# Optimization experiments

Measured on AMD Instinct MI355X. Metric: run time of the kernel, lower is better.

The kernel has to match this reference:

```python
import jax, jax.numpy as jnp
import numpy as np
import math

N = 10000      # nodes per type
DIN = 64       # input feature dim
HID = 128      # hidden_dim
HEADS = 8      # num_heads
DH = 128       # per-head dim == out_channels (PyG TransformerConv)
INNER = HEADS * DH  # 1024
L = 2          # num_layers
E = 60000      # edges per edge type
FF = 512       # 4*hidden
LN_EPS = 1e-5


def setup_inputs():
    keys = iter(jax.random.split(jax.random.key(0), 80))
    def mk(shape, std=0.05):
        return std * jax.random.normal(next(keys), shape, dtype=jnp.float32)
    inp = {}
    for t in ("job", "mach"):
        inp[f"x_{t}"] = mk((N, DIN), 1.0)
        inp[f"Win_{t}"] = mk((DIN, HID)); inp[f"bin_{t}"] = mk((HID,), 0.01)
        inp[f"pos_{t}"] = mk((N, HID)); inp[f"te_{t}"] = mk((HID,))
        inp[f"lng_{t}"] = 1.0 + mk((L, HID), 0.02); inp[f"lnb_{t}"] = mk((L, HID), 0.02)
        inp[f"W1_{t}"] = mk((L, HID, FF)); inp[f"b1_{t}"] = mk((L, FF), 0.01)
        inp[f"W2_{t}"] = mk((L, FF, HID)); inp[f"b2_{t}"] = mk((L, HID), 0.01)
        inp[f"Wout_{t}"] = mk((HID, HID)); inp[f"bout_{t}"] = mk((HID,), 0.01)
    for et in ("jm", "mj"):
        inp[f"Wq_{et}"] = mk((L, HID, INNER)); inp[f"Wk_{et}"] = mk((L, HID, INNER))
        inp[f"Wv_{et}"] = mk((L, HID, INNER)); inp[f"Ws_{et}"] = mk((L, HID, HID))
        inp[f"Wb_{et}"] = mk((L, 3 * HID, 1))
        inp[f"bq_{et}"] = mk((L, INNER), 0.01); inp[f"bk_{et}"] = mk((L, INNER), 0.01)
        inp[f"bv_{et}"] = mk((L, INNER), 0.01); inp[f"bs_{et}"] = mk((L, HID), 0.01)
        inp[f"ei_{et}"] = jax.random.randint(next(keys), (2, E), 0, N, dtype=jnp.int32)
    return inp


def _layer_norm(x, g, b):
    mu = x.mean(-1, keepdims=True)
    var = ((x - mu) ** 2).mean(-1, keepdims=True)
    return (x - mu) / jnp.sqrt(var + LN_EPS) * g + b


def _tconv(x_src, x_dst, src, dst, Wq, bq, Wk, bk, Wv, bv, Ws, bs, Wb):
    # PyG TransformerConv(heads=HEADS, out_channels=DH, concat=False, beta=True, root_weight=True)
    Nd = x_dst.shape[0]
    q = (x_dst @ Wq + bq).reshape(Nd, HEADS, DH)
    k = (x_src @ Wk + bk).reshape(-1, HEADS, DH)
    v = (x_src @ Wv + bv).reshape(-1, HEADS, DH)
    logits = jnp.einsum('ehd,ehd->eh', q[dst], k[src]) / math.sqrt(DH)  # [E,H]
    # segment softmax over edges grouped by destination node
    m = jax.ops.segment_max(logits, dst, num_segments=Nd)
    m = jnp.where(jnp.isfinite(m), m, 0.0)  # empty segments -> -inf -> 0
    ex = jnp.exp(logits - m[dst])
    den = jax.ops.segment_sum(ex, dst, num_segments=Nd)
    alpha = ex / (den[dst] + 1e-16)
    agg = jax.ops.segment_sum(alpha[:, :, None] * v[src], dst, num_segments=Nd)
    out = agg.mean(axis=1)              # concat=False -> average heads -> [Nd, DH]
    x_r = x_dst @ Ws + bs               # root/skip projection
    beta = jax.nn.sigmoid(jnp.concatenate([out, x_r, out - x_r], axis=-1) @ Wb)  # [Nd,1]
    return beta * x_r + (1.0 - beta) * out


def _ffn_block(h, new, g, b, W1, b1, W2, b2):
    r = _layer_norm(h + new, g, b)
    return r + (jax.nn.gelu(r @ W1 + b1, approximate=False) @ W2 + b2)


def _forward(x_job, Win_job, bin_job, pos_job, te_job, lng_job, lnb_job, W1_job, b1_job, W2_job, b2_job, Wout_job, bout_job, x_mach, Win_mach, bin_mach, pos_mach, te_mach, lng_mach, lnb_mach, W1_mach, b1_mach, W2_mach, b2_mach, Wout_mach, bout_mach, Wq_jm, Wk_jm, Wv_jm, Ws_jm, Wb_jm, bq_jm, bk_jm, bv_jm, bs_jm, ei_jm, Wq_mj, Wk_mj, Wv_mj, Ws_mj, Wb_mj, bq_mj, bk_mj, bv_mj, bs_mj, ei_mj):
    h_j = x_job @ Win_job + bin_job + te_job + pos_job
    h_m = x_mach @ Win_mach + bin_mach + te_mach + pos_mach
    s_jm, d_jm = ei_jm[0], ei_jm[1]  # job -> mach
    s_mj, d_mj = ei_mj[0], ei_mj[1]  # mach -> job
    for l in range(L):
        new_m = _tconv(h_j, h_m, s_jm, d_jm, Wq_jm[l], bq_jm[l], Wk_jm[l], bk_jm[l], Wv_jm[l], bv_jm[l], Ws_jm[l], bs_jm[l], Wb_jm[l])
        new_j = _tconv(h_m, h_j, s_mj, d_mj, Wq_mj[l], bq_mj[l], Wk_mj[l], bk_mj[l], Wv_mj[l], bv_mj[l], Ws_mj[l], bs_mj[l], Wb_mj[l])
        h_j = _ffn_block(h_j, new_j, lng_job[l], lnb_job[l], W1_job[l], b1_job[l], W2_job[l], b2_job[l])
        h_m = _ffn_block(h_m, new_m, lng_mach[l], lnb_mach[l], W1_mach[l], b1_mach[l], W2_mach[l], b2_mach[l])
    return jnp.stack([h_j @ Wout_job + bout_job, h_m @ Wout_mach + bout_mach], axis=0)


def reference(x_job, Win_job, bin_job, pos_job, te_job, lng_job, lnb_job, W1_job, b1_job, W2_job, b2_job, Wout_job, bout_job, x_mach, Win_mach, bin_mach, pos_mach, te_mach, lng_mach, lnb_mach, W1_mach, b1_mach, W2_mach, b2_mach, Wout_mach, bout_mach, Wq_jm, Wk_jm, Wv_jm, Ws_jm, Wb_jm, bq_jm, bk_jm, bv_jm, bs_jm, ei_jm, Wq_mj, Wk_mj, Wv_mj, Ws_mj, Wb_mj, bq_mj, bk_mj, bv_mj, bs_mj, ei_mj):
    return _forward(x_job, Win_job, bin_job, pos_job, te_job, lng_job, lnb_job, W1_job, b1_job, W2_job, b2_job, Wout_job, bout_job, x_mach, Win_mach, bin_mach, pos_mach, te_mach, lng_mach, lnb_mach, W1_mach, b1_mach, W2_mach, b2_mach, Wout_mach, bout_mach, Wq_jm, Wk_jm, Wv_jm, Ws_jm, Wb_jm, bq_jm, bk_jm, bv_jm, bs_jm, ei_jm, Wq_mj, Wk_mj, Wv_mj, Ws_mj, Wb_mj, bq_mj, bk_mj, bv_mj, bs_mj, ei_mj)
```

## Files before the change

### kernel.cpp

```cpp
#include <hip/hip_runtime.h>
#include <hip/hip_bf16.h>

#define NN 10000
#define EE 60000
#define HIDD 128
#define NH 8
#define INNERD 1024
#define FFD 512
#define KVQ 3072
#define KVQS 3200

using u16 = unsigned short;
using u32 = unsigned int;

typedef __bf16 bf16x8 __attribute__((ext_vector_type(8)));
typedef float f32x4 __attribute__((ext_vector_type(4)));

__device__ __forceinline__ float u2f(u32 u) { return __uint_as_float(u << 16); }
__device__ __forceinline__ u16 f2b(float f) {
  u32 x = __float_as_uint(f);
  return (u16)((x + 0x7fffu + ((x >> 16) & 1u)) >> 16);
}
__device__ __forceinline__ float gelu_f(float x) {
  return 0.5f * x * (1.0f + erff(x * 0.70710678118654752f));
}

__global__ void detect_k(const u32* __restrict__ xw, int* __restrict__ flag) {
  if (threadIdx.x == 0 && blockIdx.x == 0) {
    int wild = 0;
    for (int i = 0; i < 256; ++i) {
      float v = u2f(xw[i] & 0xffffu);
      if (!(fabsf(v) < 1e4f)) ++wild;
    }
    *flag = (wild > 16) ? 1 : 0;
  }
}

#define NCVT 30
struct CvtArgs { const void* src[NCVT]; int cnt[NCVT]; int ntot; };

__global__ __launch_bounds__(256) void convert_k(CvtArgs a, const int* __restrict__ flag,
                                                 float* __restrict__ dst) {
  const int i = blockIdx.x * 256 + threadIdx.x;
  if (i >= a.ntot) return;
  int t = 0, off = i;
  while (off >= a.cnt[t]) { off -= a.cnt[t]; ++t; }
  const float v = (*flag) ? ((const float*)a.src[t])[off]
                          : u2f(((const u16*)a.src[t])[off]);
  dst[i] = v;
}

struct TT { const void* s; long off; u16* d; int K; int N; };
struct TTab { TT m[28]; };

__global__ __launch_bounds__(256) void transT_k(TTab tt, const int* __restrict__ flag) {
  const TT m = tt.m[blockIdx.z];
  const int n0 = blockIdx.x * 32, k0 = blockIdx.y * 32;
  if (n0 >= m.N || k0 >= m.K) return;
  __shared__ float tile[32][33];
  const int c = threadIdx.x;
  const int f32in = *flag;
  for (int i = threadIdx.y; i < 32; i += 8) {
    const long gi = m.off + (long)(k0 + i) * m.N + n0 + c;
    tile[i][c] = f32in ? ((const float*)m.s)[gi] : u2f(((const u16*)m.s)[gi]);
  }
  __syncthreads();
  for (int i = threadIdx.y; i < 32; i += 8)
    m.d[(size_t)(n0 + i) * m.K + k0 + c] = f2b(tile[c][i]);
}

__global__ __launch_bounds__(256) void hist_k(const int* __restrict__ ei0,
                                              const int* __restrict__ ei1,
                                              int* __restrict__ hist) {
  const int e = blockIdx.x * 256 + threadIdx.x;
  if (e >= EE) return;
  const int et = blockIdx.y;
  const int* ei = et ? ei1 : ei0;
  atomicAdd(&hist[et * NN + ei[EE + e]], 1);
}

__global__ __launch_bounds__(1024) void scan2_k(const int* __restrict__ hist,
                                                int* __restrict__ rowptr,
                                                int* __restrict__ cursor) {
  const int et = blockIdx.x;
  const int* h = hist + et * NN;
  int* rp = rowptr + et * (NN + 1);
  int* cu = cursor + et * NN;
  __shared__ int wsum[16];
  __shared__ int carrySm;
  const int t = threadIdx.x, lane = t & 63, wid = t >> 6;
  if (t == 0) carrySm = 0;
  __syncthreads();
  for (int base = 0; base < NN; base += 1024) {
    const int idx = base + t;
    const int v = (idx < NN) ? h[idx] : 0;
    int x = v;
#pragma unroll
    for (int off = 1; off < 64; off <<= 1) {
      int y = __shfl_up(x, off);
      if (lane >= off) x += y;
    }
    if (lane == 63) wsum[wid] = x;
    __syncthreads();
    if (wid == 0) {
      int s = (lane < 16) ? wsum[lane] : 0;
#pragma unroll
      for (int off = 1; off < 16; off <<= 1) {
        int y = __shfl_up(s, off);
        if (lane >= off) s += y;
      }
      if (lane < 16) wsum[lane] = s;
    }
    __syncthreads();
    const int waveoff = (wid > 0) ? wsum[wid - 1] : 0;
    const int incl = x + waveoff + carrySm;
    if (idx < NN) { rp[idx] = incl - v; cu[idx] = incl - v; }
    __syncthreads();
    if (t == 1023) carrySm = incl;
    __syncthreads();
  }
  if (t == 0) rp[NN] = carrySm;
}

__global__ __launch_bounds__(256) void scat_k(const int* __restrict__ ei0,
                                              const int* __restrict__ ei1,
                                              int* __restrict__ cursor,
                                              int* __restrict__ srcs) {
  const int e = blockIdx.x * 256 + threadIdx.x;
  if (e >= EE) return;
  const int et = blockIdx.y;
  const int* ei = et ? ei1 : ei0;
  const int s = ei[e], d = ei[EE + e];
  const int pos = atomicAdd(&cursor[et * NN + d], 1);
  srcs[et * EE + pos] = s;
}

__global__ __launch_bounds__(128) void embed2_k(
    const void* __restrict__ x0, const float* __restrict__ Win0,
    const float* __restrict__ bin0, const float* __restrict__ te0,
    const void* __restrict__ pos0, float* __restrict__ h0, u16* __restrict__ h80,
    const void* __restrict__ x1, const float* __restrict__ Win1,
    const float* __restrict__ bin1, const float* __restrict__ te1,
    const void* __restrict__ pos1, float* __restrict__ h1, u16* __restrict__ h81,
    const int* __restrict__ flag) {
  const int ty = blockIdx.y;
  const void* x = ty ? x1 : x0;
  const float* Win = ty ? Win1 : Win0;
  const float* bin = ty ? bin1 : bin0;
  const float* te = ty ? te1 : te0;
  const void* pos = ty ? pos1 : pos0;
  float* h = ty ? h1 : h0;
  u16* h8 = ty ? h81 : h80;
  __shared__ float Ws[64][128];
  __shared__ float xs[16][64];
  const int f32in = *flag;
  const int j = threadIdx.x;
  const int base = blockIdx.x * 16;
  for (int i = 0; i < 64; ++i) Ws[i][j] = Win[i * 128 + j];
  for (int r = 0; r < 8; ++r) {
    int idx = r * 128 + j;
    int row = idx >> 6, k = idx & 63;
    size_t gi = (size_t)(base + row) * 64 + k;
    xs[row][k] = f32in ? ((const float*)x)[gi] : u2f(((const u16*)x)[gi]);
  }
  __syncthreads();
  float bj = bin[j] + te[j];
  for (int row = 0; row < 16; ++row) {
    size_t gi = (size_t)(base + row) * 128 + j;
    float pv = f32in ? ((const float*)pos)[gi] : u2f(((const u16*)pos)[gi]);
    float acc = bj + pv;
#pragma unroll
    for (int k = 0; k < 64; ++k) acc += xs[row][k] * Ws[k][j];
    h[(size_t)(base + row) * 128 + j] = acc;
    h8[(size_t)(base + row) * 128 + j] = f2b(acc);
  }
}

struct MG {
  const u16* A; const u16* WT;
  const float* b0; const float* b1; const float* b2; const float* b3;
  const float* add; float* Cf; u16* Cb;
};

template <int MODE>
__global__ __launch_bounds__(256) void mgemm2_k(MG g0, MG g1, int M, int N, int K) {
  const MG g = blockIdx.z ? g1 : g0;
  __shared__ __align__(16) u16 Asl[128][40];
  __shared__ __align__(16) u16 Bsl[64][40];
  const int t = threadIdx.x;
  const int lane = t & 63, wid = t >> 6;
  const int bm = blockIdx.y * 128, bn = blockIdx.x * 64;
  const int rg = lane >> 4, rr = lane & 15;
  f32x4 acc[2][4];
#pragma unroll
  for (int i = 0; i < 2; ++i)
#pragma unroll
    for (int j = 0; j < 4; ++j) acc[i][j] = (f32x4){0.f, 0.f, 0.f, 0.f};
  const int ar = t >> 1;
  const int ah = (t & 1) << 4;
  const int wr = t >> 2;
  const int wk = (t & 3) << 3;

  for (int k0 = 0; k0 < K; k0 += 32) {
    const int garow = bm + ar;
    uint4 a0 = {0,0,0,0}, a1 = {0,0,0,0};
    if (garow < M) {
      const u16* ap = g.A + (size_t)garow * K + k0 + ah;
      a0 = *reinterpret_cast<const uint4*>(ap);
      a1 = *reinterpret_cast<const uint4*>(ap + 8);
    }
    *reinterpret_cast<uint4*>(&Asl[ar][ah]) = a0;
    *reinterpret_cast<uint4*>(&Asl[ar][ah + 8]) = a1;
    const uint4 bv = *reinterpret_cast<const uint4*>(g.WT + (size_t)(bn + wr) * K + k0 + wk);
    *reinterpret_cast<uint4*>(&Bsl[wr][wk]) = bv;
    __syncthreads();
    bf16x8 af[2], bfr[4];
#pragma unroll
    for (int mi = 0; mi < 2; ++mi)
      af[mi] = *reinterpret_cast<const bf16x8*>(&Asl[wid * 32 + mi * 16 + rr][rg * 8]);
#pragma unroll
    for (int ni = 0; ni < 4; ++ni)
      bfr[ni] = *reinterpret_cast<const bf16x8*>(&Bsl[ni * 16 + rr][rg * 8]);
#pragma unroll
    for (int mi = 0; mi < 2; ++mi)
#pragma unroll
      for (int ni = 0; ni < 4; ++ni)
        acc[mi][ni] = __builtin_amdgcn_mfma_f32_16x16x32_bf16(af[mi], bfr[ni], acc[mi][ni], 0, 0, 0);
    __syncthreads();
  }
#pragma unroll
  for (int mi = 0; mi < 2; ++mi) {
#pragma unroll
    for (int ni = 0; ni < 4; ++ni) {
      const int col = bn + ni * 16 + rr;
      float bcol;
      if (MODE == 2) {
        const int seg = col >> 10;
        const float* bp = (seg == 0) ? g.b0 : ((seg == 1) ? g.b1 : ((seg == 2) ? g.b2 : g.b3));
        bcol = bp[col & 1023];
      } else {
        bcol = g.b0[col];
      }
#pragma unroll
      for (int r = 0; r < 4; ++r) {
        const int row = bm + wid * 32 + mi * 16 + rg * 4 + r;
        if (row >= M) continue;
        float v = acc[mi][ni][r] + bcol;
        if (MODE == 2) {
          if (col < KVQ) g.Cb[(size_t)row * KVQ + col] = f2b(v);
          else           g.Cf[(size_t)row * HIDD + (col - KVQ)] = v;
        } else if (MODE == 3) {
          v = gelu_f(v);
          g.Cb[(size_t)row * N + col] = f2b(v);
        } else {
          v += g.add[(size_t)row * N + col];
          g.Cf[(size_t)row * N + col] = v;
          g.Cb[(size_t)row * N + col] = f2b(v);
        }
      }
    }
  }
}

struct VG {
  const float* A; const float* B; const float* bias;
  float* Cf; u16* Cb;
};

__global__ __launch_bounds__(256) void gemm2_k(VG g0, VG g1, const int* __restrict__ oflag,
                                               int M, int N, int K) {
  const VG g = blockIdx.z ? g1 : g0;
  __shared__ __align__(16) float As[16][64];
  __shared__ __align__(16) float Bs[16][64];
  const int t = threadIdx.x;
  const int tx = t & 15, ty = t >> 4;
  const int bm = blockIdx.y * 64, bn = blockIdx.x * 64;
  float c[4][4] = {{0.f}};
  const int am = t >> 2;
  const int ak = (t & 3) << 2;
  const int bk = t >> 4;
  const int bn4 = (t & 15) << 2;
  for (int k0 = 0; k0 < K; k0 += 16) {
    float4 av = make_float4(0.f, 0.f, 0.f, 0.f);
    const int arow = bm + am;
    if (arow < M) av = *reinterpret_cast<const float4*>(g.A + (size_t)arow * K + k0 + ak);
    As[ak + 0][am] = av.x; As[ak + 1][am] = av.y;
    As[ak + 2][am] = av.z; As[ak + 3][am] = av.w;
    float4 bv = *reinterpret_cast<const float4*>(g.B + (size_t)(k0 + bk) * N + bn + bn4);
    Bs[bk][bn4 + 0] = bv.x; Bs[bk][bn4 + 1] = bv.y;
    Bs[bk][bn4 + 2] = bv.z; Bs[bk][bn4 + 3] = bv.w;
    __syncthreads();
#pragma unroll
    for (int kk = 0; kk < 16; ++kk) {
      float4 a = *reinterpret_cast<const float4*>(&As[kk][ty << 2]);
      float4 b = *reinterpret_cast<const float4*>(&Bs[kk][tx << 2]);
      c[0][0] += a.x * b.x; c[0][1] += a.x * b.y; c[0][2] += a.x * b.z; c[0][3] += a.x * b.w;
      c[1][0] += a.y * b.x; c[1][1] += a.y * b.y; c[1][2] += a.y * b.z; c[1][3] += a.y * b.w;
      c[2][0] += a.z * b.x; c[2][1] += a.z * b.y; c[2][2] += a.z * b.z; c[2][3] += a.z * b.w;
      c[3][0] += a.w * b.x; c[3][1] += a.w * b.y; c[3][2] += a.w * b.z; c[3][3] += a.w * b.w;
    }
    __syncthreads();
  }
  const int f32out = *oflag;
#pragma unroll
  for (int i = 0; i < 4; ++i) {
    const int row = bm + (ty << 2) + i;
    if (row >= M) continue;
#pragma unroll
    for (int j = 0; j < 4; ++j) {
      const int col = bn + (tx << 2) + j;
      float v = c[i][j] + g.bias[col];
      if (f32out) g.Cf[(size_t)row * N + col] = v;
      else        g.Cb[(size_t)row * N + col] = f2b(v);
    }
  }
}

struct ABL {
  const float* Wb; const float* hrow; const float* lgam; const float* lbet;
  const float* xr; float* r; u16* r8;
};

__global__ __launch_bounds__(256) void attnbl2_k(
    const u16* __restrict__ kvqJ, const u16* __restrict__ kvqM,
    const int* __restrict__ rowptr, const int* __restrict__ srcs,
    ABL bl0, ABL bl1) {
  const int et = blockIdx.y;
  const u16* kvqS = et ? kvqM : kvqJ;
  const u16* kvqD = et ? kvqJ : kvqM;
  const int* rp = rowptr + et * (NN + 1);
  const int* sr = srcs + et * EE;
  const ABL pb = et ? bl1 : bl0;
  const int d = (blockIdx.x * 256 + threadIdx.x) >> 6;
  const int lane = threadIdx.x & 63;
  const u16* qp = kvqD + (size_t)d * KVQ + 2048 + lane * 16;
  uint4 q0 = *reinterpret_cast<const uint4*>(qp);
  uint4 q1 = *reinterpret_cast<const uint4*>(qp + 8);
  float qf[16];
  {
    u32 w[8] = {q0.x, q0.y, q0.z, q0.w, q1.x, q1.y, q1.z, q1.w};
#pragma unroll
    for (int i = 0; i < 8; ++i) { qf[2*i] = u2f(w[i] & 0xffffu); qf[2*i+1] = u2f(w[i] >> 16); }
  }
  float m = -INFINITY, den = 0.f;
  float acc[16];
#pragma unroll
  for (int i = 0; i < 16; ++i) acc[i] = 0.f;
  const int beg = rp[d], end = rp[d + 1];

  auto dot8 = [&](const uint4& a, const uint4& b) -> float {
    float p = 0.f;
    const u32 w[8] = {a.x, a.y, a.z, a.w, b.x, b.y, b.z, b.w};
#pragma unroll
    for (int i = 0; i < 8; ++i) {
      p += qf[2*i] * u2f(w[i] & 0xffffu);
      p += qf[2*i+1] * u2f(w[i] >> 16);
    }
    return p;
  };
  auto wred = [&](float p) -> float {
    p += __shfl_xor(p, 1);
    p += __shfl_xor(p, 2);
    p += __shfl_xor(p, 4);
    return p * 0.088388347648318447f;
  };

  int idx = beg;
  for (; idx + 2 <= end; idx += 2) {
    const int s0 = sr[idx], s1 = sr[idx + 1];
    const u16* kp0 = kvqS + (size_t)s0 * KVQ + lane * 16;
    const u16* kp1 = kvqS + (size_t)s1 * KVQ + lane * 16;
    const uint4 a0 = *reinterpret_cast<const uint4*>(kp0);
    const uint4 a1 = *reinterpret_cast<const uint4*>(kp0 + 8);
    const uint4 av0 = *reinterpret_cast<const uint4*>(kp0 + 1024);
    const uint4 av1 = *reinterpret_cast<const uint4*>(kp0 + 1024 + 8);
    const uint4 b0 = *reinterpret_cast<const uint4*>(kp1);
    const uint4 b1 = *reinterpret_cast<const uint4*>(kp1 + 8);
    const uint4 bv0 = *reinterpret_cast<const uint4*>(kp1 + 1024);
    const uint4 bv1 = *reinterpret_cast<const uint4*>(kp1 + 1024 + 8);
    const float lg0 = wred(dot8(a0, a1));
    const float lg1 = wred(dot8(b0, b1));
    const float nm = fmaxf(m, fmaxf(lg0, lg1));
    const float cor = __expf(m - nm);
    const float p0 = __expf(lg0 - nm);
    const float p1 = __expf(lg1 - nm);
    den = den * cor + p0 + p1;
    const u32 wa[8] = {av0.x, av0.y, av0.z, av0.w, av1.x, av1.y, av1.z, av1.w};
    const u32 wb[8] = {bv0.x, bv0.y, bv0.z, bv0.w, bv1.x, bv1.y, bv1.z, bv1.w};
#pragma unroll
    for (int i = 0; i < 8; ++i) {
      acc[2*i]   = (acc[2*i]   * cor + p0 * u2f(wa[i] & 0xffffu)) + p1 * u2f(wb[i] & 0xffffu);
      acc[2*i+1] = (acc[2*i+1] * cor + p0 * u2f(wa[i] >> 16))     + p1 * u2f(wb[i] >> 16);
    }
    m = nm;
  }
  if (idx < end) {
    const int s0 = sr[idx];
    const u16* kp0 = kvqS + (size_t)s0 * KVQ + lane * 16;
    const uint4 a0 = *reinterpret_cast<const uint4*>(kp0);
    const uint4 a1 = *reinterpret_cast<const uint4*>(kp0 + 8);
    const uint4 av0 = *reinterpret_cast<const uint4*>(kp0 + 1024);
    const uint4 av1 = *reinterpret_cast<const uint4*>(kp0 + 1024 + 8);
    const float lg = wred(dot8(a0, a1));
    const float nm = fmaxf(m, lg);
    const float cor = __expf(m - nm);
    const float p = __expf(lg - nm);
    den = den * cor + p;
    const u32 w[8] = {av0.x, av0.y, av0.z, av0.w, av1.x, av1.y, av1.z, av1.w};
#pragma unroll
    for (int i = 0; i < 8; ++i) {
      acc[2*i]   = acc[2*i]   * cor + p * u2f(w[i] & 0xffffu);
      acc[2*i+1] = acc[2*i+1] * cor + p * u2f(w[i] >> 16);
    }
    m = nm;
  }

  const float inv = 0.125f / (den + 1e-16f);
  float o[16];
#pragma unroll
  for (int i = 0; i < 16; ++i) {
    float tv = acc[i] * inv;
    tv += __shfl_xor(tv, 8);
    tv += __shfl_xor(tv, 16);
    tv += __shfl_xor(tv, 32);
    o[i] = tv;
  }

  const int g8 = (lane & 7) * 16;
  float x[16], hd[16];
  {
    const float* xrp = pb.xr + (size_t)d * HIDD + g8;
    const float* hp  = pb.hrow + (size_t)d * HIDD + g8;
#pragma unroll
    for (int i = 0; i < 16; i += 4) {
      const float4 xv = *reinterpret_cast<const float4*>(xrp + i);
      const float4 hv = *reinterpret_cast<const float4*>(hp + i);
      x[i] = xv.x; x[i+1] = xv.y; x[i+2] = xv.z; x[i+3] = xv.w;
      hd[i] = hv.x; hd[i+1] = hv.y; hd[i+2] = hv.z; hd[i+3] = hv.w;
    }
  }
  float s = 0.f;
#pragma unroll
  for (int i = 0; i < 16; ++i) {
    s += o[i] * pb.Wb[g8 + i] + x[i] * pb.Wb[128 + g8 + i]
       + (o[i] - x[i]) * pb.Wb[256 + g8 + i];
  }
  s += __shfl_xor(s, 1);
  s += __shfl_xor(s, 2);
  s += __shfl_xor(s, 4);
  const float beta = 1.f / (1.f + expf(-s));
  float v[16];
  float psum = 0.f;
#pragma unroll
  for (int i = 0; i < 16; ++i) {
    v[i] = hd[i] + beta * x[i] + (1.f - beta) * o[i];
    psum += v[i];
  }
  psum += __shfl_xor(psum, 1);
  psum += __shfl_xor(psum, 2);
  psum += __shfl_xor(psum, 4);
  const float mu = psum * (1.f / 128.f);
  float pvar = 0.f;
#pragma unroll
  for (int i = 0; i < 16; ++i) {
    const float dv = v[i] - mu;
    pvar += dv * dv;
  }
  pvar += __shfl_xor(pvar, 1);
  pvar += __shfl_xor(pvar, 2);
  pvar += __shfl_xor(pvar, 4);
  const float rstd = rsqrtf(pvar * (1.f / 128.f) + 1e-5f);
  float r[16];
#pragma unroll
  for (int i = 0; i < 16; ++i)
    r[i] = (v[i] - mu) * rstd * pb.lgam[g8 + i] + pb.lbet[g8 + i];
  if (lane < 8) {
    float* rp_ = pb.r + (size_t)d * HIDD + g8;
#pragma unroll
    for (int i = 0; i < 16; i += 4)
      *reinterpret_cast<float4*>(rp_ + i) = make_float4(r[i], r[i+1], r[i+2], r[i+3]);
    u32 pk[8];
#pragma unroll
    for (int i = 0; i < 8; ++i)
      pk[i] = (u32)f2b(r[2*i]) | ((u32)f2b(r[2*i+1]) << 16);
    uint4* r8p = reinterpret_cast<uint4*>(pb.r8 + (size_t)d * HIDD + g8);
    r8p[0] = (uint4){pk[0], pk[1], pk[2], pk[3]};
    r8p[1] = (uint4){pk[4], pk[5], pk[6], pk[7]};
  }
}

extern "C" void kernel_launch(void* const* d_in, const int* in_sizes, int n_in,
                              void* d_out, int out_size, void* d_ws, size_t ws_size,
                              hipStream_t stream) {
  char* w = (char*)d_ws;
  auto carve = [&](size_t bytes) { void* p = (void*)w; w += (bytes + 255) & ~(size_t)255; return p; };
  float* h_b[2];  h_b[0] = (float*)carve((size_t)NN * HIDD * 4); h_b[1] = (float*)carve((size_t)NN * HIDD * 4);
  u16* h8_b[2];   h8_b[0] = (u16*)carve((size_t)NN * HIDD * 2);  h8_b[1] = (u16*)carve((size_t)NN * HIDD * 2);
  float* rb_b[2]; rb_b[0] = (float*)carve((size_t)NN * HIDD * 4); rb_b[1] = (float*)carve((size_t)NN * HIDD * 4);
  u16* rb8_b[2];  rb8_b[0] = (u16*)carve((size_t)NN * HIDD * 2);  rb8_b[1] = (u16*)carve((size_t)NN * HIDD * 2);
  float* xr_b[2]; xr_b[0] = (float*)carve((size_t)NN * HIDD * 4); xr_b[1] = (float*)carve((size_t)NN * HIDD * 4);
  u16* kvqJ = (u16*)carve((size_t)NN * KVQ * 2);
  u16* kvqM = (u16*)carve((size_t)NN * KVQ * 2);
  u16* mid8_b[2] = {kvqJ, kvqM};
  int* histb  = (int*)carve(2 * NN * 4);
  int* rowptr = (int*)carve(2 * (NN + 1) * 4);
  int* cursor = (int*)carve(2 * NN * 4);
  int* srcsb  = (int*)carve(2 * EE * 4);
  int* flagp  = (int*)carve(256);
  const int totCvt = 2 * 26752 + 2 * 7168;
  float* wf = (float*)carve((size_t)totCvt * 4);
  u16* wtp = (u16*)carve((size_t)(4 * KVQS * HIDD + 8 * HIDD * FFD) * 2);

  CvtArgs ca; int nc = 0; int cum = 0;
  auto addc = [&](int inIdx, int n) -> float* {
    ca.src[nc] = d_in[inIdx]; ca.cnt[nc] = n; float* p = wf + cum; cum += n; ++nc; return p;
  };
  const float *WinF[2], *binF[2], *teF[2], *lngF[2], *lnbF[2], *b1F[2], *b2F[2], *WoutF[2], *boutF[2];
  const void* x_p[2]; const void* pos_p[2];
  for (int t = 0; t < 2; ++t) {
    const int o = t * 13;
    x_p[t] = d_in[o + 0];
    WinF[t] = addc(o + 1, 64 * HIDD);
    binF[t] = addc(o + 2, HIDD);
    pos_p[t] = d_in[o + 3];
    teF[t]  = addc(o + 4, HIDD);
    lngF[t] = addc(o + 5, 2 * HIDD);
    lnbF[t] = addc(o + 6, 2 * HIDD);
    b1F[t]  = addc(o + 8, 2 * FFD);
    b2F[t]  = addc(o + 10, 2 * HIDD);
    WoutF[t] = addc(o + 11, HIDD * HIDD);
    boutF[t] = addc(o + 12, HIDD);
  }
  const float *WbF[2], *bqF[2], *bkF[2], *bvF[2], *bsF[2];
  const int* ei_e[2];
  for (int et = 0; et < 2; ++et) {
    const int o = 26 + et * 10;
    WbF[et] = addc(o + 4, 2 * 384);
    bqF[et] = addc(o + 5, 2 * INNERD);
    bkF[et] = addc(o + 6, 2 * INNERD);
    bvF[et] = addc(o + 7, 2 * INNERD);
    bsF[et] = addc(o + 8, 2 * HIDD);
    ei_e[et] = (const int*)d_in[o + 9];
  }
  ca.ntot = cum;

  TTab tt; int ntt = 0; u16* tcur = wtp;
  auto addT = [&](const void* s, long off, int K, int N, u16* dst) {
    tt.m[ntt] = {s, off, dst, K, N}; ++ntt;
  };
  u16* kvqWT[2][2];
  for (int et = 0; et < 2; ++et) {
    const int o  = 26 + et * 10;
    const int oq = 26 + (1 - et) * 10;
    for (int l = 0; l < 2; ++l) {
      u16* base = tcur; tcur += (size_t)KVQS * HIDD;
      kvqWT[et][l] = base;
      addT(d_in[o + 1],  (long)l * HIDD * INNERD, HIDD, INNERD, base);
      addT(d_in[o + 2],  (long)l * HIDD * INNERD, HIDD, INNERD, base + 1024 * HIDD);
      addT(d_in[oq + 0], (long)l * HIDD * INNERD, HIDD, INNERD, base + 2048 * HIDD);
      addT(d_in[oq + 3], (long)l * HIDD * HIDD,   HIDD, HIDD,   base + 3072 * HIDD);
    }
  }
  u16 *W1T[2][2], *W2T[2][2];
  for (int t = 0; t < 2; ++t) {
    const int o = t * 13;
    for (int l = 0; l < 2; ++l) {
      W1T[t][l] = tcur; addT(d_in[o + 7], (long)l * HIDD * FFD, HIDD, FFD, tcur); tcur += (size_t)HIDD * FFD;
      W2T[t][l] = tcur; addT(d_in[o + 9], (long)l * FFD * HIDD, FFD, HIDD, tcur); tcur += (size_t)FFD * HIDD;
    }
  }

  const dim3 blk(256);
  const int MB64 = (NN + 63) / 64;
  const int MB128 = (NN + 127) / 128;

  detect_k<<<1, 64, 0, stream>>>((const u32*)d_in[0], flagp);
  convert_k<<<(cum + 255) / 256, blk, 0, stream>>>(ca, flagp, wf);
  transT_k<<<dim3(32, 16, 24), dim3(32, 8), 0, stream>>>(tt, flagp);
  hipMemsetAsync(histb, 0, 2 * NN * 4, stream);
  hist_k<<<dim3((EE + 255) / 256, 2), blk, 0, stream>>>(ei_e[0], ei_e[1], histb);
  scan2_k<<<2, 1024, 0, stream>>>(histb, rowptr, cursor);
  scat_k<<<dim3((EE + 255) / 256, 2), blk, 0, stream>>>(ei_e[0], ei_e[1], cursor, srcsb);

  embed2_k<<<dim3(NN / 16, 2), 128, 0, stream>>>(
      x_p[0], WinF[0], binF[0], teF[0], pos_p[0], h_b[0], h8_b[0],
      x_p[1], WinF[1], binF[1], teF[1], pos_p[1], h_b[1], h8_b[1], flagp);

  for (int l = 0; l < 2; ++l) {
    MG gj = {h8_b[0], kvqWT[0][l], bkF[0] + l * INNERD, bvF[0] + l * INNERD,
             bqF[1] + l * INNERD, bsF[1] + l * HIDD, nullptr, xr_b[0], kvqJ};
    MG gm = {h8_b[1], kvqWT[1][l], bkF[1] + l * INNERD, bvF[1] + l * INNERD,
             bqF[0] + l * INNERD, bsF[0] + l * HIDD, nullptr, xr_b[1], kvqM};
    mgemm2_k<2><<<dim3(KVQS / 64, MB128, 2), blk, 0, stream>>>(gj, gm, NN, KVQS, HIDD);
    ABL bl0 = {WbF[0] + l * 384, h_b[1], lngF[1] + l * HIDD, lnbF[1] + l * HIDD,
               xr_b[1], rb_b[1], rb8_b[1]};
    ABL bl1 = {WbF[1] + l * 384, h_b[0], lngF[0] + l * HIDD, lnbF[0] + l * HIDD,
               xr_b[0], rb_b[0], rb8_b[0]};
    attnbl2_k<<<dim3(NN / 4, 2), blk, 0, stream>>>(kvqJ, kvqM, rowptr, srcsb, bl0, bl1);
    MG w1j = {rb8_b[0], W1T[0][l], b1F[0] + l * FFD, nullptr, nullptr, nullptr,
              nullptr, nullptr, mid8_b[0]};
    MG w1m = {rb8_b[1], W1T[1][l], b1F[1] + l * FFD, nullptr, nullptr, nullptr,
              nullptr, nullptr, mid8_b[1]};
    mgemm2_k<3><<<dim3(FFD / 64, MB128, 2), blk, 0, stream>>>(w1j, w1m, NN, FFD, HIDD);
    MG w2j = {mid8_b[0], W2T[0][l], b2F[0] + l * HIDD, nullptr, nullptr, nullptr,
              rb_b[0], h_b[0], h8_b[0]};
    MG w2m = {mid8_b[1], W2T[1][l], b2F[1] + l * HIDD, nullptr, nullptr, nullptr,
              rb_b[1], h_b[1], h8_b[1]};
    mgemm2_k<4><<<dim3(HIDD / 64, MB128, 2), blk, 0, stream>>>(w2j, w2m, NN, HIDD, FFD);
  }
  VG o0 = {h_b[0], WoutF[0], boutF[0], (float*)d_out, (u16*)d_out};
  VG o1 = {h_b[1], WoutF[1], boutF[1],
           (float*)d_out + (size_t)NN * HIDD, (u16*)d_out + (size_t)NN * HIDD};
  gemm2_k<<<dim3(HIDD / 64, MB64, 2), blk, 0, stream>>>(o0, o1, flagp, NN, HIDD, HIDD);
}
```

Measured before the change: 461.1 us.

## Load full K=128 tiles once in bf16 GEMMs and move output projection to MFMA

For the K=128 GEMMs (KVQ projection, W1, and the new output projection), the kernel now loads the entire A and B K-extent into shared memory in one pass with a single barrier, then runs four MFMA sub-steps, removing the per-32 K-loop synchronisation. The final fp32 scalar output GEMM is replaced by the bf16 MFMA path using a transposed Wout and the bf16 copy of h. This cuts barriers and FMA work but uses more LDS per block, which can lower occupancy, and the output projection now reads bf16 activations, which lowers precision.

Result: slower. 536.2 us (+16.3%).

```diff
diff --git a/kernel.cpp b/kernel.cpp
--- a/kernel.cpp
+++ b/kernel.cpp
@@ -179,14 +179,12 @@
 struct MG {
   const u16* A; const u16* WT;
   const float* b0; const float* b1; const float* b2; const float* b3;
-  const float* add; float* Cf; u16* Cb;
+  const float* add; float* Cf; u16* Cb; const int* oflag;
 };
 
 template <int MODE>
 __global__ __launch_bounds__(256) void mgemm2_k(MG g0, MG g1, int M, int N, int K) {
   const MG g = blockIdx.z ? g1 : g0;
-  __shared__ __align__(16) u16 Asl[128][40];
-  __shared__ __align__(16) u16 Bsl[64][40];
   const int t = threadIdx.x;
   const int lane = t & 63, wid = t >> 6;
   const int bm = blockIdx.y * 128, bn = blockIdx.x * 64;
@@ -196,38 +194,77 @@
   for (int i = 0; i < 2; ++i)
 #pragma unroll
     for (int j = 0; j < 4; ++j) acc[i][j] = (f32x4){0.f, 0.f, 0.f, 0.f};
-  const int ar = t >> 1;
-  const int ah = (t & 1) << 4;
-  const int wr = t >> 2;
-  const int wk = (t & 3) << 3;
-
-  for (int k0 = 0; k0 < K; k0 += 32) {
+
+  if constexpr (MODE != 4) {
+    __shared__ __align__(16) u16 Asl[128][136];
+    __shared__ __align__(16) u16 Bsl[64][136];
+    const int ar = t >> 1, ah = (t & 1) << 6;
     const int garow = bm + ar;
-    uint4 a0 = {0,0,0,0}, a1 = {0,0,0,0};
-    if (garow < M) {
-      const u16* ap = g.A + (size_t)garow * K + k0 + ah;
-      a0 = *reinterpret_cast<const uint4*>(ap);
-      a1 = *reinterpret_cast<const uint4*>(ap + 8);
-    }
-    *reinterpret_cast<uint4*>(&Asl[ar][ah]) = a0;
-    *reinterpret_cast<uint4*>(&Asl[ar][ah + 8]) = a1;
-    const uint4 bv = *reinterpret_cast<const uint4*>(g.WT + (size_t)(bn + wr) * K + k0 + wk);
-    *reinterpret_cast<uint4*>(&Bsl[wr][wk]) = bv;
+#pragma unroll
+    for (int j = 0; j < 8; ++j) {
+      uint4 av = {0, 0, 0, 0};
+      if (garow < M) av = *reinterpret_cast<const uint4*>(g.A + (size_t)garow * 128 + ah + j * 8);
+      *reinterpret_cast<uint4*>(&Asl[ar][ah + j * 8]) = av;
+    }
+    const int wr = t >> 2, wk = (t & 3) << 5;
+#pragma unroll
+    for (int j = 0; j < 4; ++j) {
+      const uint4 bv = *reinterpret_cast<const uint4*>(g.WT + (size_t)(bn + wr) * 128 + wk + j * 8);
+      *reinterpret_cast<uint4*>(&Bsl[wr][wk + j * 8]) = bv;
+    }
     __syncthreads();
-    bf16x8 af[2], bfr[4];
-#pragma unroll
-    for (int mi = 0; mi < 2; ++mi)
-      af[mi] = *reinterpret_cast<const bf16x8*>(&Asl[wid * 32 + mi * 16 + rr][rg * 8]);
-#pragma unroll
-    for (int ni = 0; ni < 4; ++ni)
-      bfr[ni] = *reinterpret_cast<const bf16x8*>(&Bsl[ni * 16 + rr][rg * 8]);
-#pragma unroll
-    for (int mi = 0; mi < 2; ++mi)
+#pragma unroll
+    for (int kk = 0; kk < 4; ++kk) {
+      bf16x8 af[2], bfr[4];
+#pragma unroll
+      for (int mi = 0; mi < 2; ++mi)
+        af[mi] = *reinterpret_cast<const bf16x8*>(&Asl[wid * 32 + mi * 16 + rr][rg * 8 + kk * 32]);
 #pragma unroll
       for (int ni = 0; ni < 4; ++ni)
-        acc[mi][ni] = __builtin_amdgcn_mfma_f32_16x16x32_bf16(af[mi], bfr[ni], acc[mi][ni], 0, 0, 0);
-    __syncthreads();
-  }
+        bfr[ni] = *reinterpret_cast<const bf16x8*>(&Bsl[ni * 16 + rr][rg * 8 + kk * 32]);
+#pragma unroll
+      for (int mi = 0; mi < 2; ++mi)
+#pragma unroll
+        for (int ni = 0; ni < 4; ++ni)
+          acc[mi][ni] = __builtin_amdgcn_mfma_f32_16x16x32_bf16(af[mi], bfr[ni], acc[mi][ni], 0, 0, 0);
+    }
+  } else {
+    __shared__ __align__(16) u16 Asl[128][40];
+    __shared__ __align__(16) u16 Bsl[64][40];
+    const int ar = t >> 1;
+    const int ah = (t & 1) << 4;
+    const int wr = t >> 2;
+    const int wk = (t & 3) << 3;
+    for (int k0 = 0; k0 < K; k0 += 32) {
+      const int garow = bm + ar;
+      uint4 a0 = {0, 0, 0, 0}, a1 = {0, 0, 0, 0};
+      if (garow < M) {
+        const u16* ap = g.A + (size_t)garow * K + k0 + ah;
+        a0 = *reinterpret_cast<const uint4*>(ap);
+        a1 = *reinterpret_cast<const uint4*>(ap + 8);
+      }
+      *reinterpret_cast<uint4*>(&Asl[ar][ah]) = a0;
+      *reinterpret_cast<uint4*>(&Asl[ar][ah + 8]) = a1;
+      const uint4 bv = *reinterpret_cast<const uint4*>(g.WT + (size_t)(bn + wr) * K + k0 + wk);
+      *reinterpret_cast<uint4*>(&Bsl[wr][wk]) = bv;
+      __syncthreads();
+      bf16x8 af[2], bfr[4];
+#pragma unroll
+      for (int mi = 0; mi < 2; ++mi)
+        af[mi] = *reinterpret_cast<const bf16x8*>(&Asl[wid * 32 + mi * 16 + rr][rg * 8]);
+#pragma unroll
+      for (int ni = 0; ni < 4; ++ni)
+        bfr[ni] = *reinterpret_cast<const bf16x8*>(&Bsl[ni * 16 + rr][rg * 8]);
+#pragma unroll
+      for (int mi = 0; mi < 2; ++mi)
+#pragma unroll
+        for (int ni = 0; ni < 4; ++ni)
+          acc[mi][ni] = __builtin_amdgcn_mfma_f32_16x16x32_bf16(af[mi], bfr[ni], acc[mi][ni], 0, 0, 0);
+      __syncthreads();
+    }
+  }
+
+  const int f32o = (MODE == 5) ? *g.oflag : 0;
 #pragma unroll
   for (int mi = 0; mi < 2; ++mi) {
 #pragma unroll
@@ -252,66 +289,15 @@
         } else if (MODE == 3) {
           v = gelu_f(v);
           g.Cb[(size_t)row * N + col] = f2b(v);
-        } else {
+        } else if (MODE == 4) {
           v += g.add[(size_t)row * N + col];
           g.Cf[(size_t)row * N + col] = v;
           g.Cb[(size_t)row * N + col] = f2b(v);
+        } else {
+          if (f32o) g.Cf[(size_t)row * N + col] = v;
+          else      g.Cb[(size_t)row * N + col] = f2b(v);
         }
       }
-    }
-  }
-}
-
-struct VG {
-  const float* A; const float* B; const float* bias;
-  float* Cf; u16* Cb;
-};
-
-__global__ __launch_bounds__(256) void gemm2_k(VG g0, VG g1, const int* __restrict__ oflag,
-                                               int M, int N, int K) {
-  const VG g = blockIdx.z ? g1 : g0;
-  __shared__ __align__(16) float As[16][64];
-  __shared__ __align__(16) float Bs[16][64];
-  const int t = threadIdx.x;
-  const int tx = t & 15, ty = t >> 4;
-  const int bm = blockIdx.y * 64, bn = blockIdx.x * 64;
-  float c[4][4] = {{0.f}};
-  const int am = t >> 2;
-  const int ak = (t & 3) << 2;
-  const int bk = t >> 4;
-  const int bn4 = (t & 15) << 2;
-  for (int k0 = 0; k0 < K; k0 += 16) {
-    float4 av = make_float4(0.f, 0.f, 0.f, 0.f);
-    const int arow = bm + am;
-    if (arow < M) av = *reinterpret_cast<const float4*>(g.A + (size_t)arow * K + k0 + ak);
-    As[ak + 0][am] = av.x; As[ak + 1][am] = av.y;
-    As[ak + 2][am] = av.z; As[ak + 3][am] = av.w;
-    float4 bv = *reinterpret_cast<const float4*>(g.B + (size_t)(k0 + bk) * N + bn + bn4);
-    Bs[bk][bn4 + 0] = bv.x; Bs[bk][bn4 + 1] = bv.y;
-    Bs[bk][bn4 + 2] = bv.z; Bs[bk][bn4 + 3] = bv.w;
-    __syncthreads();
-#pragma unroll
-    for (int kk = 0; kk < 16; ++kk) {
-      float4 a = *reinterpret_cast<const float4*>(&As[kk][ty << 2]);
-      float4 b = *reinterpret_cast<const float4*>(&Bs[kk][tx << 2]);
-      c[0][0] += a.x * b.x; c[0][1] += a.x * b.y; c[0][2] += a.x * b.z; c[0][3] += a.x * b.w;
-      c[1][0] += a.y * b.x; c[1][1] += a.y * b.y; c[1][2] += a.y * b.z; c[1][3] += a.y * b.w;
-      c[2][0] += a.z * b.x; c[2][1] += a.z * b.y; c[2][2] += a.z * b.z; c[2][3] += a.z * b.w;
-      c[3][0] += a.w * b.x; c[3][1] += a.w * b.y; c[3][2] += a.w * b.z; c[3][3] += a.w * b.w;
-    }
-    __syncthreads();
-  }
-  const int f32out = *oflag;
-#pragma unroll
-  for (int i = 0; i < 4; ++i) {
-    const int row = bm + (ty << 2) + i;
-    if (row >= M) continue;
-#pragma unroll
-    for (int j = 0; j < 4; ++j) {
-      const int col = bn + (tx << 2) + j;
-      float v = c[i][j] + g.bias[col];
-      if (f32out) g.Cf[(size_t)row * N + col] = v;
-      else        g.Cb[(size_t)row * N + col] = f2b(v);
     }
   }
 }
@@ -509,7 +495,7 @@
   int* flagp  = (int*)carve(256);
   const int totCvt = 2 * 26752 + 2 * 7168;
   float* wf = (float*)carve((size_t)totCvt * 4);
-  u16* wtp = (u16*)carve((size_t)(4 * KVQS * HIDD + 8 * HIDD * FFD) * 2);
+  u16* wtp = (u16*)carve((size_t)(4 * KVQS * HIDD + 8 * HIDD * FFD + 2 * HIDD * HIDD) * 2);
 
   CvtArgs ca; int nc = 0; int cum = 0;
   auto addc = [&](int inIdx, int n) -> float* {
@@ -561,7 +547,7 @@
       addT(d_in[oq + 3], (long)l * HIDD * HIDD,   HIDD, HIDD,   base + 3072 * HIDD);
     }
   }
-  u16 *W1T[2][2], *W2T[2][2];
+  u16 *W1T[2][2], *W2T[2][2], *WoutT[2];
   for (int t = 0; t < 2; ++t) {
     const int o = t * 13;
     for (int l = 0; l < 2; ++l) {
@@ -569,14 +555,17 @@
       W2T[t][l] = tcur; addT(d_in[o + 9], (long)l * FFD * HIDD, FFD, HIDD, tcur); tcur += (size_t)FFD * HIDD;
     }
   }
+  for (int t = 0; t < 2; ++t) {
+    const int o = t * 13;
+    WoutT[t] = tcur; addT(d_in[o + 11], 0, HIDD, HIDD, tcur); tcur += (size_t)HIDD * HIDD;
+  }
 
   const dim3 blk(256);
-  const int MB64 = (NN + 63) / 64;
   const int MB128 = (NN + 127) / 128;
 
   detect_k<<<1, 64, 0, stream>>>((const u32*)d_in[0], flagp);
   convert_k<<<(cum + 255) / 256, blk, 0, stream>>>(ca, flagp, wf);
-  transT_k<<<dim3(32, 16, 24), dim3(32, 8), 0, stream>>>(tt, flagp);
+  transT_k<<<dim3(32, 16, 26), dim3(32, 8), 0, stream>>>(tt, flagp);
   hipMemsetAsync(histb, 0, 2 * NN * 4, stream);
   hist_k<<<dim3((EE + 255) / 256, 2), blk, 0, stream>>>(ei_e[0], ei_e[1], histb);
   scan2_k<<<2, 1024, 0, stream>>>(histb, rowptr, cursor);
@@ -588,9 +577,9 @@
 
   for (int l = 0; l < 2; ++l) {
     MG gj = {h8_b[0], kvqWT[0][l], bkF[0] + l * INNERD, bvF[0] + l * INNERD,
-             bqF[1] + l * INNERD, bsF[1] + l * HIDD, nullptr, xr_b[0], kvqJ};
+             bqF[1] + l * INNERD, bsF[1] + l * HIDD, nullptr, xr_b[0], kvqJ, nullptr};
     MG gm = {h8_b[1], kvqWT[1][l], bkF[1] + l * INNERD, bvF[1] + l * INNERD,
-             bqF[0] + l * INNERD, bsF[0] + l * HIDD, nullptr, xr_b[1], kvqM};
+             bqF[0] + l * INNERD, bsF[0] + l * HIDD, nullptr, xr_b[1], kvqM, nullptr};
     mgemm2_k<2><<<dim3(KVQS / 64, MB128, 2), blk, 0, stream>>>(gj, gm, NN, KVQS, HIDD);
     ABL bl0 = {WbF[0] + l * 384, h_b[1], lngF[1] + l * HIDD, lnbF[1] + l * HIDD,
                xr_b[1], rb_b[1], rb8_b[1]};
@@ -598,18 +587,19 @@
                xr_b[0], rb_b[0], rb8_b[0]};
     attnbl2_k<<<dim3(NN / 4, 2), blk, 0, stream>>>(kvqJ, kvqM, rowptr, srcsb, bl0, bl1);
     MG w1j = {rb8_b[0], W1T[0][l], b1F[0] + l * FFD, nullptr, nullptr, nullptr,
-              nullptr, nullptr, mid8_b[0]};
+              nullptr, nullptr, mid8_b[0], nullptr};
     MG w1m = {rb8_b[1], W1T[1][l], b1F[1] + l * FFD, nullptr, nullptr, nullptr,
-              nullptr, nullptr, mid8_b[1]};
+              nullptr, nullptr, mid8_b[1], nullptr};
     mgemm2_k<3><<<dim3(FFD / 64, MB128, 2), blk, 0, stream>>>(w1j, w1m, NN, FFD, HIDD);
     MG w2j = {mid8_b[0], W2T[0][l], b2F[0] + l * HIDD, nullptr, nullptr, nullptr,
-              rb_b[0], h_b[0], h8_b[0]};
+              rb_b[0], h_b[0], h8_b[0], nullptr};
     MG w2m = {mid8_b[1], W2T[1][l], b2F[1] + l * HIDD, nullptr, nullptr, nullptr,
-              rb_b[1], h_b[1], h8_b[1]};
+              rb_b[1], h_b[1], h8_b[1], nullptr};
     mgemm2_k<4><<<dim3(HIDD / 64, MB128, 2), blk, 0, stream>>>(w2j, w2m, NN, HIDD, FFD);
   }
-  VG o0 = {h_b[0], WoutF[0], boutF[0], (float*)d_out, (u16*)d_out};
-  VG o1 = {h_b[1], WoutF[1], boutF[1],
-           (float*)d_out + (size_t)NN * HIDD, (u16*)d_out + (size_t)NN * HIDD};
-  gemm2_k<<<dim3(HIDD / 64, MB64, 2), blk, 0, stream>>>(o0, o1, flagp, NN, HIDD, HIDD);
-}
+  MG o0 = {h8_b[0], WoutT[0], boutF[0], nullptr, nullptr, nullptr,
+           nullptr, (float*)d_out, (u16*)d_out, flagp};
+  MG o1 = {h8_b[1], WoutT[1], boutF[1], nullptr, nullptr, nullptr,
+           nullptr, (float*)d_out + (size_t)NN * HIDD, (u16*)d_out + (size_t)NN * HIDD, flagp};
+  mgemm2_k<5><<<dim3(HIDD / 64, MB128, 2), blk, 0, stream>>>(o0, o1, NN, HIDD, HIDD);
+}
```
